# Optimization experiments

Hardware: AMD Instinct MI355X
Metric: run time of the kernel (lower is better)

The kernel has to match this reference:

```python
import jax, jax.numpy as jnp
import numpy as np

D_MODEL = 1024
N_HEAD = 8      # KV heads
N_QUERY = 4     # query groups per KV head
D_HEAD = D_MODEL // (N_HEAD * N_QUERY)  # 32
KV_DIM = D_HEAD * N_HEAD                # 256
BATCH, SEQ = 4, 1024
BASE = 10000.0


def _rope(x):
    """Interleaved RoPE as in the torch module. theta denominator is always
    d_model/2 = 512 (layer-level), even when applied to the 256-dim key."""
    d = x.shape[-1]
    d2 = d // 2
    dm2 = D_MODEL // 2
    theta = BASE ** (-jnp.arange(dm2, dtype=jnp.float32) / dm2)  # [512]
    pos = jnp.arange(x.shape[-2], dtype=jnp.float32)
    ang = pos[:, None] * theta[None, :d2]  # [S, d2]
    cos, sin = jnp.cos(ang), jnp.sin(ang)
    xe, xo = x[..., ::2], x[..., 1::2]
    out = jnp.stack([xe * cos - xo * sin, xo * cos + xe * sin], axis=-1)
    return out.reshape(x.shape)


def setup_inputs() -> dict:
    key = jax.random.key(0)
    ks = jax.random.split(key, 6)
    x = jax.random.normal(ks[0], (BATCH, SEQ, D_MODEL), dtype=jnp.float32)
    s = 0.02
    Wq = jax.random.normal(ks[1], (D_MODEL, D_MODEL), dtype=jnp.float32) * s
    Wk = jax.random.normal(ks[2], (KV_DIM, D_MODEL), dtype=jnp.float32) * s
    Wv = jax.random.normal(ks[3], (KV_DIM, D_MODEL), dtype=jnp.float32) * s
    Wo = jax.random.normal(ks[4], (D_MODEL, D_MODEL), dtype=jnp.float32) * s
    bo = jnp.zeros((D_MODEL,), dtype=jnp.float32)
    # causal mask: True = masked out
    causal = jnp.triu(jnp.ones((SEQ, SEQ), dtype=bool), k=1)
    mask = jnp.broadcast_to(causal[None, None], (BATCH, 1, SEQ, SEQ))
    return {"x": x, "Wq": Wq, "Wk": Wk, "Wv": Wv, "Wo": Wo, "bo": bo, "mask": mask}


def reference(x, Wq, Wk, Wv, Wo, bo, mask):
    n_b, n_seq, _ = x.shape
    q = _rope(x @ Wq.T)                 # [B,S,1024]
    k = _rope(x @ Wk.T)                 # [B,S,256]
    v = x @ Wv.T                        # [B,S,256]
    # head split; KV heads repeat-interleaved n_query times to match query heads
    qh = q.reshape(n_b, n_seq, N_QUERY * N_HEAD, D_HEAD).transpose(0, 2, 1, 3)
    kh = jnp.repeat(k.reshape(n_b, n_seq, N_HEAD, D_HEAD), N_QUERY, axis=2).transpose(0, 2, 1, 3)
    vh = jnp.repeat(v.reshape(n_b, n_seq, N_HEAD, D_HEAD), N_QUERY, axis=2).transpose(0, 2, 1, 3)
    scale = 1.0 / jnp.sqrt(jnp.float32(D_HEAD))
    scores = jnp.einsum('bhqd,bhkd->bhqk', qh, kh) * scale
    scores = jnp.where(mask, jnp.float32(-1e9), scores)
    probs = jax.nn.softmax(scores, axis=-1)
    probs = jnp.where(mask, jnp.float32(0.0), probs)
    out = jnp.einsum('bhqk,bhkd->bqhd', probs, vh)  # [B,S,32,32]
    out = out.reshape(n_b, n_seq, D_MODEL)
    return out @ Wo.T + bo
```

## Files before the change

### kernel.cpp

```cpp
#include <hip/hip_runtime.h>
#include <hip/hip_bf16.h>

typedef __attribute__((ext_vector_type(8))) short short8;
typedef __attribute__((ext_vector_type(4))) short short4v;
typedef __attribute__((ext_vector_type(4))) float float4v;

#define DEV __device__ __forceinline__

constexpr int SEQ = 1024;
constexpr int DM  = 1024;
constexpr int KVD = 256;
constexpr int MTOK = 4096;

constexpr float QSCALE = 0.25503487660444f;


DEV void load_lds16(const void* g, void* l) {
  __builtin_amdgcn_global_load_lds(
      (const __attribute__((address_space(1))) unsigned int*)g,
      (__attribute__((address_space(3))) unsigned int*)l, 16, 0, 0);
}

DEV unsigned short f2bf(float f) {
  unsigned int u = __float_as_uint(f);
  u += 0x7fffu + ((u >> 16) & 1u);
  return (unsigned short)(u >> 16);
}

DEV float fexp2(float x) {
  float y;
  asm("v_exp_f32 %0, %1" : "=v"(y) : "v"(x));
  return y;
}

DEV unsigned int cvtpk(float lo, float hi) {
  unsigned int r;
  asm("v_cvt_pk_bf16_f32 %0, %1, %2" : "=v"(r) : "v"(lo), "v"(hi));
  return r;
}

#if __has_builtin(__builtin_amdgcn_mfma_f32_16x16x16bf16_1k)
DEV float4v mfma16(short4v a, short4v b, float4v c) {
  return __builtin_amdgcn_mfma_f32_16x16x16bf16_1k(a, b, c, 0, 0, 0);
}
#else
DEV float4v mfma16(short4v a, short4v b, float4v c) {
  asm("v_mfma_f32_16x16x16_bf16 %0, %1, %2, %0" : "+v"(c) : "v"(a), "v"(b));
  return c;
}
#endif

#define WAIT_VM(N)  asm volatile("s_waitcnt vmcnt(" #N ")" ::: "memory")
#define WAIT_LG(N)  asm volatile("s_waitcnt lgkmcnt(" #N ")" ::: "memory")
#define WAIT_LGKM0  asm volatile("s_waitcnt lgkmcnt(0)" ::: "memory")
#define SBAR0       __builtin_amdgcn_sched_barrier(0)


__global__ __launch_bounds__(256)
void prep_kernel(const float* __restrict__ x,  const float* __restrict__ Wq,
                 const float* __restrict__ Wk, const float* __restrict__ Wv,
                 const float* __restrict__ Wo,
                 unsigned short* __restrict__ xb, unsigned short* __restrict__ Wqkvb,
                 unsigned short* __restrict__ Wob,
                 float* __restrict__ rc, float* __restrict__ rs)
{
  const int NX  = (MTOK*DM)/4;
  const int NWQ = (DM*DM)/4;
  const int NWK = (KVD*DM)/4;
  const int NCONV = NX + NWQ + 2*NWK + NWQ;
  int id = blockIdx.x*256 + threadIdx.x;
  if (id < NCONV) {
    const float* src; unsigned short* dst; int u;
    if      (id < NX)            { src = x;  dst = xb;                     u = id; }
    else if (id < NX+NWQ)        { src = Wq; dst = Wqkvb;                  u = id-NX; }
    else if (id < NX+NWQ+NWK)    { src = Wk; dst = Wqkvb + DM*DM;          u = id-(NX+NWQ); }
    else if (id < NX+NWQ+2*NWK)  { src = Wv; dst = Wqkvb + DM*DM+KVD*DM;   u = id-(NX+NWQ+NWK); }
    else                         { src = Wo; dst = Wob;                    u = id-(NX+NWQ+2*NWK); }
    float4 v = ((const float4*)src)[u];
    ushort4 o;
    o.x = f2bf(v.x); o.y = f2bf(v.y); o.z = f2bf(v.z); o.w = f2bf(v.w);
    ((ushort4*)dst)[u] = o;
  } else {
    int id2 = id - NCONV;
    if (id2 < SEQ*512) {
      int pos = id2 >> 9, i = id2 & 511;
      float theta = exp2f((float)i * (-13.287712379549449f/512.0f));
      float ang = (float)pos * theta;
      float sv, cv; sincosf(ang, &sv, &cv);
      rc[id2] = cv; rs[id2] = sv;
    }
  }
}


template<int MODE, int GY>
__global__ __launch_bounds__(256)
void gemm_nt(const unsigned short* __restrict__ A, const unsigned short* __restrict__ Bw,
             unsigned short* __restrict__ outQ, unsigned short* __restrict__ outK,
             unsigned short* __restrict__ outVt, float* __restrict__ outF,
             const float* __restrict__ bias,
             const float* __restrict__ rc, const float* __restrict__ rs)
{
  __shared__ __align__(16) unsigned short As[2][128*64];
  __shared__ __align__(16) unsigned short Bs[2][64*64];
  const int tid = threadIdx.x;
  const int w  = tid >> 6, l = tid & 63;
  const int lg = l >> 4, ll = l & 15;
  const int wr = w >> 1, wc = w & 1;

  const int bid = (int)blockIdx.x;
  const int f   = (bid & 7) * (4*GY) + (bid >> 3);
  const int brow = (f / GY) * 128, bcol = (f % GY) * 64;

  float4v acc[4][2];
#pragma unroll
  for (int i = 0; i < 4; ++i)
#pragma unroll
    for (int j = 0; j < 2; ++j) acc[i][j] = (float4v){0.f,0.f,0.f,0.f};

  auto stage = [&](int kt, int cur) {
#pragma unroll
    for (int blk = 0; blk < 4; ++blk) {
      int cid = blk*256 + w*64 + l;
      int row = cid >> 3, c = cid & 7;
      int cg = c ^ (row & 7);
      load_lds16(A + (size_t)(brow+row)*DM + kt*64 + cg*8,
                 &As[cur][(blk*256 + w*64)*8]);
    }
#pragma unroll
    for (int blk = 0; blk < 2; ++blk) {
      int cid = blk*256 + w*64 + l;
      int row = cid >> 3, c = cid & 7;
      int cg = c ^ (row & 7);
      load_lds16(Bw + (size_t)(bcol+row)*DM + kt*64 + cg*8,
                 &Bs[cur][(blk*256 + w*64)*8]);
    }
  };

  stage(0, 0); stage(1, 1);
#pragma unroll 1
  for (int kt = 0; kt < 16; ++kt) {
    const int cur = kt & 1;
    if (kt < 15) { WAIT_VM(6); }
    else         { WAIT_VM(0); }
    __builtin_amdgcn_s_barrier();

    short8 af[2][4], bf[2][2];
#pragma unroll
    for (int mi = 0; mi < 4; ++mi) {
      int row = wr*64 + mi*16 + ll;
      af[0][mi] = *(const short8*)&As[cur][row*64 + ((lg ^ (row & 7)) << 3)];
    }
#pragma unroll
    for (int ni = 0; ni < 2; ++ni) {
      int col = wc*32 + ni*16 + ll;
      bf[0][ni] = *(const short8*)&Bs[cur][col*64 + ((lg ^ (col & 7)) << 3)];
    }
    SBAR0;
#pragma unroll
    for (int mi = 0; mi < 4; ++mi) {
      int row = wr*64 + mi*16 + ll;
      af[1][mi] = *(const short8*)&As[cur][row*64 + (((4 + lg) ^ (row & 7)) << 3)];
    }
#pragma unroll
    for (int ni = 0; ni < 2; ++ni) {
      int col = wc*32 + ni*16 + ll;
      bf[1][ni] = *(const short8*)&Bs[cur][col*64 + (((4 + lg) ^ (col & 7)) << 3)];
    }
    WAIT_LG(6);
    SBAR0;
    __builtin_amdgcn_s_setprio(1);
#pragma unroll
    for (int mi = 0; mi < 4; ++mi)
#pragma unroll
      for (int ni = 0; ni < 2; ++ni)
        acc[mi][ni] = __builtin_amdgcn_mfma_f32_16x16x32_bf16(af[0][mi], bf[0][ni], acc[mi][ni], 0,0,0);
    __builtin_amdgcn_s_setprio(0);
    SBAR0;
    WAIT_LGKM0;
    SBAR0;
    __builtin_amdgcn_s_barrier();

    if (kt + 2 < 16) stage(kt + 2, cur);

    __builtin_amdgcn_s_setprio(1);
#pragma unroll
    for (int mi = 0; mi < 4; ++mi)
#pragma unroll
      for (int ni = 0; ni < 2; ++ni)
        acc[mi][ni] = __builtin_amdgcn_mfma_f32_16x16x32_bf16(af[1][mi], bf[1][ni], acc[mi][ni], 0,0,0);
    __builtin_amdgcn_s_setprio(0);
  }

#pragma unroll
  for (int mi = 0; mi < 4; ++mi)
#pragma unroll
    for (int ni = 0; ni < 2; ++ni)
#pragma unroll
      for (int r = 0; r < 4; ++r) {
        int m = brow + wr*64 + mi*16 + lg*4 + r;
        int n = bcol + wc*32 + ni*16 + ll;
        float v = acc[mi][ni][r];
        if constexpr (MODE == 0) {
          float p = __shfl_xor(v, 1);
          if (n < DM) {
            int pos = m & (SEQ-1);
            int i = n >> 1;
            float ct = rc[pos*512 + i], st = rs[pos*512 + i];
            v = (n & 1) ? (v*ct + p*st) : (v*ct - p*st);
            outQ[(size_t)m*DM + n] = f2bf(v * QSCALE);
          } else if (n < DM + KVD) {
            int nk = n - DM;
            int pos = m & (SEQ-1);
            int i = nk >> 1;
            float ct = rc[pos*512 + i], st = rs[pos*512 + i];
            v = (nk & 1) ? (v*ct + p*st) : (v*ct - p*st);
            outK[(size_t)m*KVD + nk] = f2bf(v);
          } else {
            int nv = n - DM - KVD;
            outVt[((size_t)(m >> 10)*KVD + nv)*SEQ + (m & (SEQ-1))] = f2bf(v);
          }
        } else {
          outF[(size_t)m*DM + n] = v + bias[n];
        }
      }
}


__global__ __launch_bounds__(256, 4)
void attn_kernel(const unsigned short* __restrict__ Qb, const unsigned short* __restrict__ Kb,
                 const unsigned short* __restrict__ Vtb, unsigned short* __restrict__ Ob)
{
  __shared__ __align__(16) unsigned short Kl[2][32*64];
  __shared__ __align__(16) unsigned short Vl[2][32*64];
  const int tid = threadIdx.x;
  const int w  = tid >> 6, l = tid & 63;
  const int lg = l >> 4, ll = l & 15;
  const int hk = (int)blockIdx.x & 7, b = (int)blockIdx.x >> 3;
  const int h  = hk*4 + w;

  auto stage = [&](int kvt, int bi) {
    const int kv0 = kvt*64;
    {
      int row = tid >> 3, slot = tid & 7;
      int sp = slot ^ (row & 7);
      int kv = row*2 + (sp >> 2), c = sp & 3;
      load_lds16(&Kb[((size_t)b*SEQ + kv0 + kv)*KVD + hk*32 + c*8],
                 &Kl[bi][(w*64)*8]);
    }
    {
      int d = tid >> 3, c = tid & 7, cl = c ^ (d & 7);
      load_lds16(&Vtb[((size_t)b*KVD + hk*32 + d)*SEQ + kv0 + cl*8],
                 &Vl[bi][(w*64)*8]);
    }
  };

#pragma unroll 1
  for (int ph = 0; ph < 2; ++ph) {
    const int qt = ph ? (int)blockIdx.y : 63 - (int)blockIdx.y;
    const int nt = (qt + 4) >> 2;
    const int q0 = qt*16;

    short8 qf = *(const short8*)&Qb[((size_t)b*SEQ + q0 + ll)*DM + h*32 + (lg<<3)];

    float4v o[2];
    float lrow = 0.f;
    o[0] = (float4v){0,0,0,0}; o[1] = (float4v){0,0,0,0};

    WAIT_VM(0);
    stage(0, 0);
    if (1 < nt) stage(1, 1);

#pragma unroll 2
    for (int kvt = 0; kvt < nt; ++kvt) {
      const int bi = kvt & 1;
      if (kvt + 1 < nt) { WAIT_VM(2); }
      else              { WAIT_VM(0); }
      __builtin_amdgcn_s_barrier();

      short8 kf[4];
#pragma unroll
      for (int ni = 0; ni < 4; ++ni) {
        int row = ni*8 + (ll >> 1);
        int slot = (((ll & 1) << 2) + lg) ^ (row & 7);
        kf[ni] = *(const short8*)&Kl[bi][row*64 + slot*8];
      }
      short4v vf[2][4];
#pragma unroll
      for (int df = 0; df < 2; ++df) {
        int d = df*16 + ll;
#pragma unroll
        for (int ni = 0; ni < 4; ++ni) {
          int ch = (ni*2 + (lg >> 1)) ^ (d & 7);
          vf[df][ni] = *(const short4v*)&Vl[bi][d*64 + (ch << 3) + ((lg & 1) << 2)];
        }
      }
      WAIT_LGKM0;
      SBAR0;
      __builtin_amdgcn_s_barrier();

      if (kvt + 2 < nt) stage(kvt + 2, bi);

      float sc[4][4];
      __builtin_amdgcn_s_setprio(1);
#pragma unroll
      for (int ni = 0; ni < 4; ++ni) {
        float4v s = __builtin_amdgcn_mfma_f32_16x16x32_bf16(kf[ni], qf,
                       (float4v){0,0,0,0}, 0,0,0);
#pragma unroll
        for (int r = 0; r < 4; ++r) sc[ni][r] = s[r];
      }
      __builtin_amdgcn_s_setprio(0);

      if (kvt == nt-1) {
        int q = q0 + ll;
#pragma unroll
        for (int ni = 0; ni < 4; ++ni)
#pragma unroll
          for (int r = 0; r < 4; ++r) {
            int kv = kvt*64 + ni*16 + lg*4 + r;
            if (kv > q) sc[ni][r] = -1e30f;
          }
      }

      float s0 = 0.f;
      short4v pf[4];
#pragma unroll
      for (int ni = 0; ni < 4; ++ni) {
        float p0 = fexp2(sc[ni][0]);
        float p1 = fexp2(sc[ni][1]);
        float p2 = fexp2(sc[ni][2]);
        float p3 = fexp2(sc[ni][3]);
        s0 += (p0 + p1) + (p2 + p3);
        union { unsigned int u[2]; short4v s4; } cv;
        cv.u[0] = cvtpk(p0, p1); cv.u[1] = cvtpk(p2, p3);
        pf[ni] = cv.s4;
      }
      lrow += s0;

      __builtin_amdgcn_s_setprio(1);
#pragma unroll
      for (int df = 0; df < 2; ++df)
#pragma unroll
        for (int ni = 0; ni < 4; ++ni)
          o[df] = mfma16(vf[df][ni], pf[ni], o[df]);
      __builtin_amdgcn_s_setprio(0);
    }

    float s = lrow;
    s += __shfl_xor(s, 16);
    s += __shfl_xor(s, 32);
    float inv = 1.f / s;
    size_t tok = (size_t)b*SEQ + q0 + ll;
#pragma unroll
    for (int df = 0; df < 2; ++df) {
      short4v sv;
#pragma unroll
      for (int r = 0; r < 4; ++r) sv[r] = (short)f2bf(o[df][r] * inv);
      *(short4v*)&Ob[tok*DM + h*32 + df*16 + lg*4] = sv;
    }
  }
}


extern "C" void kernel_launch(void* const* d_in, const int* in_sizes, int n_in,
                              void* d_out, int out_size, void* d_ws, size_t ws_size,
                              hipStream_t stream)
{
  const float* x  = (const float*)d_in[0];
  const float* Wq = (const float*)d_in[1];
  const float* Wk = (const float*)d_in[2];
  const float* Wv = (const float*)d_in[3];
  const float* Wo = (const float*)d_in[4];
  const float* bo = (const float*)d_in[5];
  float* out = (float*)d_out;

  char* ws = (char*)d_ws;
  const size_t MB = 1u << 20;
  unsigned short* xb    = (unsigned short*)(ws + 0*MB);
  unsigned short* Wqkvb = (unsigned short*)(ws + 8*MB);
  unsigned short* Wob   = (unsigned short*)(ws + 11*MB);
  float*          rc    = (float*)(ws + 13*MB);
  float*          rs    = (float*)(ws + 15*MB);
  unsigned short* Qb    = (unsigned short*)(ws + 17*MB);
  unsigned short* Kb    = (unsigned short*)(ws + 25*MB);
  unsigned short* Vt    = (unsigned short*)(ws + 27*MB);
  unsigned short* Ob    = (unsigned short*)(ws + 29*MB);
  if (ws_size < 37*MB) return;

  {
    const int total = 1703936 + SEQ*512;
    const int blocks = (total + 255) / 256;
    prep_kernel<<<blocks, 256, 0, stream>>>(x, Wq, Wk, Wv, Wo, xb, Wqkvb, Wob, rc, rs);
  }
  gemm_nt<0, 24><<<dim3(768), 256, 0, stream>>>(xb, Wqkvb, Qb, Kb, Vt, nullptr, nullptr, rc, rs);
  attn_kernel<<<dim3(32, 32), 256, 0, stream>>>(Qb, Kb, Vt, Ob);
  gemm_nt<2, 16><<<dim3(512), 256, 0, stream>>>(Ob, Wob, nullptr, nullptr, nullptr, out, bo, rc, rs);
}
```

Before: 79.10 us.

## Load K and V fragments directly from global memory, dropping LDS staging

The attention kernel no longer stages K and V tiles through double-buffered shared memory with barriers. Each wave now reads its MFMA fragments straight from global memory, with K fragments software-prefetched one tile ahead through register ping-pong. This removes LDS traffic and block-wide barriers. In exchange, the four waves of a block each read the same K/V data separately, the V reads are narrow 8-byte loads, and global latency is only partly hidden.

Measured after the change: 146.4 us. +85.1%, slower.

```diff
diff --git a/kernel.cpp b/kernel.cpp
--- a/kernel.cpp
+++ b/kernel.cpp
@@ -231,29 +231,14 @@
 void attn_kernel(const unsigned short* __restrict__ Qb, const unsigned short* __restrict__ Kb,
                  const unsigned short* __restrict__ Vtb, unsigned short* __restrict__ Ob)
 {
-  __shared__ __align__(16) unsigned short Kl[2][32*64];
-  __shared__ __align__(16) unsigned short Vl[2][32*64];
   const int tid = threadIdx.x;
   const int w  = tid >> 6, l = tid & 63;
   const int lg = l >> 4, ll = l & 15;
   const int hk = (int)blockIdx.x & 7, b = (int)blockIdx.x >> 3;
   const int h  = hk*4 + w;
 
-  auto stage = [&](int kvt, int bi) {
-    const int kv0 = kvt*64;
-    {
-      int row = tid >> 3, slot = tid & 7;
-      int sp = slot ^ (row & 7);
-      int kv = row*2 + (sp >> 2), c = sp & 3;
-      load_lds16(&Kb[((size_t)b*SEQ + kv0 + kv)*KVD + hk*32 + c*8],
-                 &Kl[bi][(w*64)*8]);
-    }
-    {
-      int d = tid >> 3, c = tid & 7, cl = c ^ (d & 7);
-      load_lds16(&Vtb[((size_t)b*KVD + hk*32 + d)*SEQ + kv0 + cl*8],
-                 &Vl[bi][(w*64)*8]);
-    }
-  };
+  const unsigned short* Kh = Kb  + ((size_t)b*SEQ + ll)*KVD + hk*32 + (lg<<3);
+  const unsigned short* Vh = Vtb + ((size_t)b*KVD + hk*32 + ll)*SEQ + (lg<<2);
 
 #pragma unroll 1
   for (int ph = 0; ph < 2; ++ph) {
@@ -267,39 +252,19 @@
     float lrow = 0.f;
     o[0] = (float4v){0,0,0,0}; o[1] = (float4v){0,0,0,0};
 
-    WAIT_VM(0);
-    stage(0, 0);
-    if (1 < nt) stage(1, 1);
-
-#pragma unroll 2
-    for (int kvt = 0; kvt < nt; ++kvt) {
-      const int bi = kvt & 1;
-      if (kvt + 1 < nt) { WAIT_VM(2); }
-      else              { WAIT_VM(0); }
-      __builtin_amdgcn_s_barrier();
-
-      short8 kf[4];
-#pragma unroll
-      for (int ni = 0; ni < 4; ++ni) {
-        int row = ni*8 + (ll >> 1);
-        int slot = (((ll & 1) << 2) + lg) ^ (row & 7);
-        kf[ni] = *(const short8*)&Kl[bi][row*64 + slot*8];
-      }
+    auto ldK = [&](short8 (&kf)[4], int kvt) {
+#pragma unroll
+      for (int ni = 0; ni < 4; ++ni)
+        kf[ni] = *(const short8*)&Kh[(size_t)(kvt*64 + ni*16)*KVD];
+    };
+
+    auto compute = [&](const short8 (&kf)[4], int kvt) {
       short4v vf[2][4];
 #pragma unroll
-      for (int df = 0; df < 2; ++df) {
-        int d = df*16 + ll;
-#pragma unroll
-        for (int ni = 0; ni < 4; ++ni) {
-          int ch = (ni*2 + (lg >> 1)) ^ (d & 7);
-          vf[df][ni] = *(const short4v*)&Vl[bi][d*64 + (ch << 3) + ((lg & 1) << 2)];
-        }
-      }
-      WAIT_LGKM0;
-      SBAR0;
-      __builtin_amdgcn_s_barrier();
-
-      if (kvt + 2 < nt) stage(kvt + 2, bi);
+      for (int df = 0; df < 2; ++df)
+#pragma unroll
+        for (int ni = 0; ni < 4; ++ni)
+          vf[df][ni] = *(const short4v*)&Vh[(size_t)(df*16)*SEQ + kvt*64 + ni*16];
 
       float sc[4][4];
       __builtin_amdgcn_s_setprio(1);
@@ -345,6 +310,18 @@
         for (int ni = 0; ni < 4; ++ni)
           o[df] = mfma16(vf[df][ni], pf[ni], o[df]);
       __builtin_amdgcn_s_setprio(0);
+    };
+
+    short8 kfA[4], kfB[4];
+    ldK(kfA, 0);
+    int kvt = 0;
+    while (true) {
+      if (kvt + 1 < nt) ldK(kfB, kvt+1);
+      compute(kfA, kvt);
+      ++kvt; if (kvt >= nt) break;
+      if (kvt + 1 < nt) ldK(kfA, kvt+1);
+      compute(kfB, kvt);
+      ++kvt; if (kvt >= nt) break;
     }
 
     float s = lrow;
```
